# Optimization experiments

Measured on AMD Instinct MI355X. Metric: run time of the kernel, lower is better.

Reference implementation:

```python
import jax, jax.numpy as jnp
import numpy as np

# Module config (matches init_kwargs)
N_HEADS = 16
HEAD = 64
SEQ = 4096          # single prefill sequence (cu_seqlens_k = [0, SEQ])
BS = 64             # block_size (both q and k blocks)
LOCAL = 8           # local_blocks
VERT = 8            # vert_stride
NB = SEQ // BS      # number of blocks along seq
SLIDE = max(1, VERT // N_HEADS)  # get_head_sliding_step(16, 8, homo_head=False) -> 1
SM_SCALE = 1.0 / float(np.sqrt(HEAD))


def _build_layout():
    """Per-head block-sparse layout: causal + (local OR strided-vertical) blocks,
    padded to a fixed max nnz per row (CSR rows -> padded col indices + valid mask)."""
    h = np.arange(N_HEADS)[:, None, None]
    i = np.arange(NB)[None, :, None]
    j = np.arange(NB)[None, None, :]
    mask = (j <= i) & (((i - j) < LOCAL) | (((j + h * SLIDE + 1) % VERT) == 0))
    max_nnz = int(mask.sum(-1).max())
    cols = np.zeros((N_HEADS, NB, max_nnz), np.int32)
    valid = np.zeros((N_HEADS, NB, max_nnz), bool)
    for hh in range(N_HEADS):
        for ii in range(NB):
            c = np.nonzero(mask[hh, ii])[0]
            cols[hh, ii, :len(c)] = c
            valid[hh, ii, :len(c)] = True
    return cols, valid, max_nnz

_COLS_NP, _VALID_NP, MAX_NNZ = _build_layout()
COLS = jnp.asarray(_COLS_NP)    # [H, NB, NNZ] k-block ids (padded with 0)
VALID = jnp.asarray(_VALID_NP)  # [H, NB, NNZ] padding mask


def setup_inputs() -> dict:
    key = jax.random.key(0)
    kq, kk, kv = jax.random.split(key, 3)
    q = jax.random.normal(kq, (SEQ, N_HEADS, HEAD), jnp.float32)
    k = jax.random.normal(kk, (SEQ, N_HEADS, HEAD), jnp.float32)
    v = jax.random.normal(kv, (SEQ, N_HEADS, HEAD), jnp.float32)
    cu_seqlens_k = jnp.array([0, SEQ], jnp.int32)
    return {"q": q, "k": k, "v": v, "cu_seqlens_k": cu_seqlens_k}


def _attn(q, k, v):
    # [T, H, D] -> [H, NB, BS, D]
    qb = q.transpose(1, 0, 2).reshape(N_HEADS, NB, BS, HEAD)
    kb = k.transpose(1, 0, 2).reshape(N_HEADS, NB, BS, HEAD)
    vb = v.transpose(1, 0, 2).reshape(N_HEADS, NB, BS, HEAD)
    gather = jax.vmap(lambda x, c: x[c])  # per-head block gather
    kg = gather(kb, COLS)  # [H, NB, NNZ, BS, D]
    vg = gather(vb, COLS)  # [H, NB, NNZ, BS, D]
    # block-sparse scores: [H, NB(q blk), BS(m), NNZ(n), BS(j)]
    scores = jnp.einsum('himd,hinjd->himnj', qb, kg) * SM_SCALE
    qpos = jnp.arange(NB)[:, None] * BS + jnp.arange(BS)[None, :]   # [NB, BS]
    kpos = COLS[..., None] * BS + jnp.arange(BS)                    # [H, NB, NNZ, BS]
    allow = VALID[:, :, None, :, None] & (
        qpos[None, :, :, None, None] >= kpos[:, :, None, :, :])
    scores = jnp.where(allow, scores, -jnp.inf)
    p = jax.nn.softmax(scores.reshape(N_HEADS, NB, BS, MAX_NNZ * BS), axis=-1)
    p = p.reshape(N_HEADS, NB, BS, MAX_NNZ, BS)
    out = jnp.einsum('himnj,hinjd->himd', p, vg)
    return out.reshape(N_HEADS, SEQ, HEAD).transpose(1, 0, 2)  # [T, H, D]


def reference(q, k, v, cu_seqlens_k):
    # single-sequence prefill: past_len = 0, q_len == k_len == SEQ
    return _attn(q, k, v)
```

## Files before the change

### kernel.cpp

```cpp
#include <hip/hip_runtime.h>
#include <hip/hip_bf16.h>
#include <math.h>


#define NHEADS 16
#define HDIM   64
#define NBLK   64
#define SEQLEN 4096
#define KP     72
#define NEGBIG (-1.0e30f)

typedef __attribute__((ext_vector_type(8))) short bf16x8;
typedef __attribute__((ext_vector_type(4))) float f32x4;

__device__ __forceinline__ short f2bf(float x) {
    union { float f; unsigned u; } c; c.f = x;
    unsigned u = c.u;
    return (short)((u + 0x7FFFu + ((u >> 16) & 1u)) >> 16);
}
__device__ __forceinline__ short f2bf_trunc(float x) {
    union { float f; unsigned u; } c; c.f = x;
    return (short)(c.u >> 16);
}

__device__ __forceinline__ void load_lds16(const short* g, const short* l) {
    __builtin_amdgcn_global_load_lds(
        (const __attribute__((address_space(1))) void*)g,
        (__attribute__((address_space(3))) void*)l, 16, 0, 0);
}

__device__ __forceinline__ void drain_then_sync() {
    asm volatile("s_waitcnt vmcnt(0)" ::: "memory");
    __syncthreads();
}

__global__ __launch_bounds__(256)
void prep_kernel(const float* __restrict__ k, const float* __restrict__ v,
                 short* __restrict__ kt, short* __restrict__ vt) {
    __shared__ short tile[64 * KP];
    const int b = blockIdx.x;
    const int h = b >> 6, jb = b & 63;
    const int tid = threadIdx.x;

    #pragma unroll
    for (int it = 0; it < 4; ++it) {
        int e = it * 1024 + tid * 4;
        int key = e >> 6, d0 = e & 63;
        float4 f = *(const float4*)(v + ((size_t)(jb * 64 + key) * NHEADS + h) * HDIM + d0);
        tile[(d0 + 0) * KP + key] = f2bf(f.x);
        tile[(d0 + 1) * KP + key] = f2bf(f.y);
        tile[(d0 + 2) * KP + key] = f2bf(f.z);
        tile[(d0 + 3) * KP + key] = f2bf(f.w);
    }
    __syncthreads();
    short* vtile = vt + (size_t)b * 4096;
    #pragma unroll
    for (int ii = 0; ii < 2; ++ii) {
        int idx = ii * 256 + tid;
        int d = idx >> 3, gsw = idx & 7;
        int g = gsw ^ (d & 7);
        bf16x8 val;
        #pragma unroll
        for (int j = 0; j < 8; ++j) {
            int s   = g * 8 + j;
            int key = (s & 32) | (((s >> 2) & 1) << 4) | (((s >> 3) & 3) << 2) | (s & 3);
            val[j]  = tile[d * KP + key];
        }
        *(bf16x8*)(vtile + (size_t)idx * 8) = val;
    }
    short* ktile = kt + (size_t)b * 4096;
    #pragma unroll
    for (int ii = 0; ii < 2; ++ii) {
        int idx = ii * 256 + tid;
        int r = idx >> 3, g = idx & 7;
        const float* src = k + ((size_t)(jb * 64 + r) * NHEADS + h) * HDIM + g * 8;
        float4 f0 = *(const float4*)src;
        float4 f1 = *(const float4*)(src + 4);
        bf16x8 a;
        a[0]=f2bf(f0.x); a[1]=f2bf(f0.y); a[2]=f2bf(f0.z); a[3]=f2bf(f0.w);
        a[4]=f2bf(f1.x); a[5]=f2bf(f1.y); a[6]=f2bf(f1.z); a[7]=f2bf(f1.w);
        int G = r * 8 + (g ^ (r & 7));
        *(bf16x8*)(ktile + (size_t)G * 8) = a;
    }
}

__global__ __launch_bounds__(256, 4)
void attn_kernel(const short* __restrict__ kt, const short* __restrict__ vt,
                 const float* __restrict__ q, float* __restrict__ out) {
    __shared__ short kv[2 * 8192];

    const int b    = blockIdx.x;
    const int h    = ((b & 7) << 1) | ((b >> 3) & 1);
    const int idx  = b >> 4;
    const int qi   = (idx & 1) ? (63 - (idx >> 1)) : (idx >> 1);
    const int tid  = threadIdx.x;
    const int stripe = tid >> 6;
    const int lane = tid & 63;
    const int l16  = lane & 15;
    const int quad = lane >> 4;

    const int row0 = qi * 64 + stripe * 16;

    const float SC = 0.125f * 1.4426950408889634f;
    const float* qrow = q + ((size_t)(row0 + l16) * NHEADS + h) * HDIM;
    bf16x8 a_q[2];
    #pragma unroll
    for (int kk = 0; kk < 2; ++kk) {
        const float* src = qrow + kk * 32 + quad * 8;
        float4 f0 = *(const float4*)(src);
        float4 f1 = *(const float4*)(src + 4);
        bf16x8 a;
        a[0]=f2bf(f0.x*SC); a[1]=f2bf(f0.y*SC); a[2]=f2bf(f0.z*SC); a[3]=f2bf(f0.w*SC);
        a[4]=f2bf(f1.x*SC); a[5]=f2bf(f1.y*SC); a[6]=f2bf(f1.z*SC); a[7]=f2bf(f1.w*SC);
        a_q[kk] = a;
    }

    bf16x8 ones;
    #pragma unroll
    for (int j = 0; j < 8; ++j) ones[j] = (short)0x3F80;

    f32x4 o[4];
    #pragma unroll
    for (int nt = 0; nt < 4; ++nt) o[nt] = (f32x4){0.f,0.f,0.f,0.f};
    f32x4 lacc = (f32x4){0.f,0.f,0.f,0.f};

    const short* kth = kt + (size_t)(h * 64) * 4096;
    const short* vth = vt + (size_t)(h * 64) * 4096;

    const int j0  = (7 - h) & 7;
    const int l0  = (qi > 7) ? (qi - 7) : 0;
    const int nv  = (j0 < l0) ? ((l0 - j0 + 7) >> 3) : 0;
    const int T   = nv + (qi - l0 + 1);

    const int r7   = l16 & 7;
    const int gk0  = (quad ^ r7) * 8;
    const int gk1  = gk0 ^ 32;
    const int rowb = l16 * 64;
    const int qrl  = stripe * 16 + l16;

    {
        const int jb0 = (0 < nv) ? j0 : l0;
        const short* ktb = kth + (size_t)jb0 * 4096;
        const short* vtb = vth + (size_t)jb0 * 4096;
        load_lds16(ktb + (size_t)tid * 8,         &kv[stripe * 512]);
        load_lds16(ktb + (size_t)(tid + 256) * 8, &kv[2048 + stripe * 512]);
        load_lds16(vtb + (size_t)tid * 8,         &kv[4096 + stripe * 512]);
        load_lds16(vtb + (size_t)(tid + 256) * 8, &kv[6144 + stripe * 512]);
    }

    for (int t = 0; t < T; ++t) {
        drain_then_sync();

        if (t + 1 < T) {
            const int jn = (t + 1 < nv) ? (j0 + 8 * (t + 1)) : (l0 + (t + 1 - nv));
            const int bo = ((t + 1) & 1) * 8192;
            const short* ktb = kth + (size_t)jn * 4096;
            const short* vtb = vth + (size_t)jn * 4096;
            load_lds16(ktb + (size_t)tid * 8,         &kv[bo + stripe * 512]);
            load_lds16(ktb + (size_t)(tid + 256) * 8, &kv[bo + 2048 + stripe * 512]);
            load_lds16(vtb + (size_t)tid * 8,         &kv[bo + 4096 + stripe * 512]);
            load_lds16(vtb + (size_t)(tid + 256) * 8, &kv[bo + 6144 + stripe * 512]);
        }

        const short* kb = &kv[(t & 1) * 8192];
        const short* vb = kb + 4096;
        const bool diag = (t == T - 1);

        __builtin_amdgcn_s_setprio(1);

        f32x4 s[4];
        #pragma unroll
        for (int nt = 0; nt < 4; ++nt) {
            bf16x8 k0 = *(const bf16x8*)&kb[nt * 1024 + rowb + gk0];
            bf16x8 k1 = *(const bf16x8*)&kb[nt * 1024 + rowb + gk1];
            f32x4 acc = (f32x4){0.f, 0.f, 0.f, 0.f};
            acc = __builtin_amdgcn_mfma_f32_16x16x32_bf16(k0, a_q[0], acc, 0, 0, 0);
            acc = __builtin_amdgcn_mfma_f32_16x16x32_bf16(k1, a_q[1], acc, 0, 0, 0);
            s[nt] = acc;
        }

        short pb[4][4];
        #pragma unroll
        for (int nt = 0; nt < 4; ++nt) {
            #pragma unroll
            for (int r = 0; r < 4; ++r) {
                const int keyl = nt * 16 + quad * 4 + r;
                float raw = s[nt][r];
                raw = (diag && (keyl > qrl)) ? NEGBIG : raw;
                float pv = __builtin_amdgcn_exp2f(raw);
                pb[nt][r] = f2bf_trunc(pv);
            }
        }

        bf16x8 a_p0, a_p1;
        a_p0[0]=pb[0][0]; a_p0[1]=pb[0][1]; a_p0[2]=pb[0][2]; a_p0[3]=pb[0][3];
        a_p0[4]=pb[1][0]; a_p0[5]=pb[1][1]; a_p0[6]=pb[1][2]; a_p0[7]=pb[1][3];
        a_p1[0]=pb[2][0]; a_p1[1]=pb[2][1]; a_p1[2]=pb[2][2]; a_p1[3]=pb[2][3];
        a_p1[4]=pb[3][0]; a_p1[5]=pb[3][1]; a_p1[6]=pb[3][2]; a_p1[7]=pb[3][3];

        #pragma unroll
        for (int nt = 0; nt < 4; ++nt) {
            bf16x8 v0 = *(const bf16x8*)&vb[nt * 1024 + rowb + gk0];
            bf16x8 v1 = *(const bf16x8*)&vb[nt * 1024 + rowb + gk1];
            o[nt] = __builtin_amdgcn_mfma_f32_16x16x32_bf16(a_p0, v0, o[nt], 0, 0, 0);
            o[nt] = __builtin_amdgcn_mfma_f32_16x16x32_bf16(a_p1, v1, o[nt], 0, 0, 0);
        }
        lacc = __builtin_amdgcn_mfma_f32_16x16x32_bf16(a_p0, ones, lacc, 0, 0, 0);
        lacc = __builtin_amdgcn_mfma_f32_16x16x32_bf16(a_p1, ones, lacc, 0, 0, 0);

        __builtin_amdgcn_s_setprio(0);
    }

    #pragma unroll
    for (int r = 0; r < 4; ++r) {
        const float invr = 1.0f / lacc[r];
        int trow = row0 + quad * 4 + r;
        float* orow = out + ((size_t)trow * NHEADS + h) * HDIM;
        #pragma unroll
        for (int nt = 0; nt < 4; ++nt)
            orow[nt * 16 + l16] = o[nt][r] * invr;
    }
}

extern "C" void kernel_launch(void* const* d_in, const int* in_sizes, int n_in,
                              void* d_out, int out_size, void* d_ws, size_t ws_size,
                              hipStream_t stream) {
    const float* q = (const float*)d_in[0];
    const float* k = (const float*)d_in[1];
    const float* v = (const float*)d_in[2];
    float* out = (float*)d_out;

    const size_t tileBytes = (size_t)NHEADS * NBLK * 4096 * sizeof(short);
    short* kt = (short*)d_ws;
    short* vt = (short*)((char*)d_ws + tileBytes);
    prep_kernel<<<dim3(NHEADS * NBLK), dim3(256), 0, stream>>>(k, v, kt, vt);
    attn_kernel<<<dim3(1024), dim3(256), 0, stream>>>(kt, vt, q, out);
}
```

Measured before the change: 110.8 us.

## Split attention tile 2x2 across waves with LDS reduction of partial outputs

Each of the four waves now handles 32 query rows and half of the 64 keys of every block, instead of 16 query rows and all keys. Each wave loads half as many K and V fragments from LDS per block and reuses each one across two query row groups. Partial outputs and row sums from the two key halves are added through LDS in an epilogue. The price is more accumulator registers per wave, extra barriers, and a final reduction in which only half the waves write the output.

```diff
diff --git a/kernel.cpp b/kernel.cpp
--- a/kernel.cpp
+++ b/kernel.cpp
@@ -87,42 +87,51 @@
 __global__ __launch_bounds__(256, 4)
 void attn_kernel(const short* __restrict__ kt, const short* __restrict__ vt,
                  const float* __restrict__ q, float* __restrict__ out) {
-    __shared__ short kv[2 * 8192];
+    __shared__ __align__(16) short kv[2 * 8192];
 
     const int b    = blockIdx.x;
     const int h    = ((b & 7) << 1) | ((b >> 3) & 1);
     const int idx  = b >> 4;
     const int qi   = (idx & 1) ? (63 - (idx >> 1)) : (idx >> 1);
     const int tid  = threadIdx.x;
-    const int stripe = tid >> 6;
+    const int wave = tid >> 6;
+    const int ih   = wave >> 1;
+    const int jh   = wave & 1;
     const int lane = tid & 63;
     const int l16  = lane & 15;
     const int quad = lane >> 4;
 
-    const int row0 = qi * 64 + stripe * 16;
+    const int rowbase = qi * 64 + ih * 32;
 
     const float SC = 0.125f * 1.4426950408889634f;
-    const float* qrow = q + ((size_t)(row0 + l16) * NHEADS + h) * HDIM;
-    bf16x8 a_q[2];
-    #pragma unroll
-    for (int kk = 0; kk < 2; ++kk) {
-        const float* src = qrow + kk * 32 + quad * 8;
-        float4 f0 = *(const float4*)(src);
-        float4 f1 = *(const float4*)(src + 4);
-        bf16x8 a;
-        a[0]=f2bf(f0.x*SC); a[1]=f2bf(f0.y*SC); a[2]=f2bf(f0.z*SC); a[3]=f2bf(f0.w*SC);
-        a[4]=f2bf(f1.x*SC); a[5]=f2bf(f1.y*SC); a[6]=f2bf(f1.z*SC); a[7]=f2bf(f1.w*SC);
-        a_q[kk] = a;
+    bf16x8 a_q[2][2];
+    #pragma unroll
+    for (int rg = 0; rg < 2; ++rg) {
+        const float* qrow = q + ((size_t)(rowbase + rg * 16 + l16) * NHEADS + h) * HDIM;
+        #pragma unroll
+        for (int kk = 0; kk < 2; ++kk) {
+            const float* src = qrow + kk * 32 + quad * 8;
+            float4 f0 = *(const float4*)(src);
+            float4 f1 = *(const float4*)(src + 4);
+            bf16x8 a;
+            a[0]=f2bf(f0.x*SC); a[1]=f2bf(f0.y*SC); a[2]=f2bf(f0.z*SC); a[3]=f2bf(f0.w*SC);
+            a[4]=f2bf(f1.x*SC); a[5]=f2bf(f1.y*SC); a[6]=f2bf(f1.z*SC); a[7]=f2bf(f1.w*SC);
+            a_q[rg][kk] = a;
+        }
     }
 
     bf16x8 ones;
     #pragma unroll
     for (int j = 0; j < 8; ++j) ones[j] = (short)0x3F80;
 
-    f32x4 o[4];
-    #pragma unroll
-    for (int nt = 0; nt < 4; ++nt) o[nt] = (f32x4){0.f,0.f,0.f,0.f};
-    f32x4 lacc = (f32x4){0.f,0.f,0.f,0.f};
+    f32x4 o[2][4];
+    f32x4 lacc[2];
+    #pragma unroll
+    for (int rg = 0; rg < 2; ++rg) {
+        lacc[rg] = (f32x4){0.f,0.f,0.f,0.f};
+        #pragma unroll
+        for (int ntd = 0; ntd < 4; ++ntd) o[rg][ntd] = (f32x4){0.f,0.f,0.f,0.f};
+    }
 
     const short* kth = kt + (size_t)(h * 64) * 4096;
     const short* vth = vt + (size_t)(h * 64) * 4096;
@@ -135,17 +144,18 @@
     const int r7   = l16 & 7;
     const int gk0  = (quad ^ r7) * 8;
     const int gk1  = gk0 ^ 32;
+    const int gv   = (((jh << 2) | quad) ^ r7) * 8;
     const int rowb = l16 * 64;
-    const int qrl  = stripe * 16 + l16;
+    const int krow0 = (jh * 32) * 64;
 
     {
         const int jb0 = (0 < nv) ? j0 : l0;
         const short* ktb = kth + (size_t)jb0 * 4096;
         const short* vtb = vth + (size_t)jb0 * 4096;
-        load_lds16(ktb + (size_t)tid * 8,         &kv[stripe * 512]);
-        load_lds16(ktb + (size_t)(tid + 256) * 8, &kv[2048 + stripe * 512]);
-        load_lds16(vtb + (size_t)tid * 8,         &kv[4096 + stripe * 512]);
-        load_lds16(vtb + (size_t)(tid + 256) * 8, &kv[6144 + stripe * 512]);
+        load_lds16(ktb + (size_t)tid * 8,         &kv[wave * 512]);
+        load_lds16(ktb + (size_t)(tid + 256) * 8, &kv[2048 + wave * 512]);
+        load_lds16(vtb + (size_t)tid * 8,         &kv[4096 + wave * 512]);
+        load_lds16(vtb + (size_t)(tid + 256) * 8, &kv[6144 + wave * 512]);
     }
 
     for (int t = 0; t < T; ++t) {
@@ -156,10 +166,10 @@
             const int bo = ((t + 1) & 1) * 8192;
             const short* ktb = kth + (size_t)jn * 4096;
             const short* vtb = vth + (size_t)jn * 4096;
-            load_lds16(ktb + (size_t)tid * 8,         &kv[bo + stripe * 512]);
-            load_lds16(ktb + (size_t)(tid + 256) * 8, &kv[bo + 2048 + stripe * 512]);
-            load_lds16(vtb + (size_t)tid * 8,         &kv[bo + 4096 + stripe * 512]);
-            load_lds16(vtb + (size_t)(tid + 256) * 8, &kv[bo + 6144 + stripe * 512]);
+            load_lds16(ktb + (size_t)tid * 8,         &kv[bo + wave * 512]);
+            load_lds16(ktb + (size_t)(tid + 256) * 8, &kv[bo + 2048 + wave * 512]);
+            load_lds16(vtb + (size_t)tid * 8,         &kv[bo + 4096 + wave * 512]);
+            load_lds16(vtb + (size_t)(tid + 256) * 8, &kv[bo + 6144 + wave * 512]);
         }
 
         const short* kb = &kv[(t & 1) * 8192];
@@ -168,57 +178,98 @@
 
         __builtin_amdgcn_s_setprio(1);
 
-        f32x4 s[4];
-        #pragma unroll
-        for (int nt = 0; nt < 4; ++nt) {
-            bf16x8 k0 = *(const bf16x8*)&kb[nt * 1024 + rowb + gk0];
-            bf16x8 k1 = *(const bf16x8*)&kb[nt * 1024 + rowb + gk1];
-            f32x4 acc = (f32x4){0.f, 0.f, 0.f, 0.f};
-            acc = __builtin_amdgcn_mfma_f32_16x16x32_bf16(k0, a_q[0], acc, 0, 0, 0);
-            acc = __builtin_amdgcn_mfma_f32_16x16x32_bf16(k1, a_q[1], acc, 0, 0, 0);
-            s[nt] = acc;
-        }
-
-        short pb[4][4];
-        #pragma unroll
-        for (int nt = 0; nt < 4; ++nt) {
+        bf16x8 kf0[2], kf1[2];
+        #pragma unroll
+        for (int kg = 0; kg < 2; ++kg) {
+            kf0[kg] = *(const bf16x8*)&kb[krow0 + kg * 1024 + rowb + gk0];
+            kf1[kg] = *(const bf16x8*)&kb[krow0 + kg * 1024 + rowb + gk1];
+        }
+        f32x4 s[2][2];
+        #pragma unroll
+        for (int kg = 0; kg < 2; ++kg) {
+            #pragma unroll
+            for (int rg = 0; rg < 2; ++rg) {
+                f32x4 acc = (f32x4){0.f, 0.f, 0.f, 0.f};
+                acc = __builtin_amdgcn_mfma_f32_16x16x32_bf16(kf0[kg], a_q[rg][0], acc, 0, 0, 0);
+                acc = __builtin_amdgcn_mfma_f32_16x16x32_bf16(kf1[kg], a_q[rg][1], acc, 0, 0, 0);
+                s[kg][rg] = acc;
+            }
+        }
+
+        bf16x8 vf[4];
+        #pragma unroll
+        for (int ntd = 0; ntd < 4; ++ntd)
+            vf[ntd] = *(const bf16x8*)&vb[ntd * 1024 + rowb + gv];
+
+        short pb[2][2][4];
+        #pragma unroll
+        for (int kg = 0; kg < 2; ++kg) {
+            #pragma unroll
+            for (int rg = 0; rg < 2; ++rg) {
+                #pragma unroll
+                for (int r = 0; r < 4; ++r) {
+                    const int keyl = jh * 32 + kg * 16 + quad * 4 + r;
+                    const int qrl  = ih * 32 + rg * 16 + l16;
+                    float raw = s[kg][rg][r];
+                    raw = (diag && (keyl > qrl)) ? NEGBIG : raw;
+                    float pv = __builtin_amdgcn_exp2f(raw);
+                    pb[kg][rg][r] = f2bf_trunc(pv);
+                }
+            }
+        }
+
+        bf16x8 a_p[2];
+        #pragma unroll
+        for (int rg = 0; rg < 2; ++rg) {
+            bf16x8 a;
+            a[0]=pb[0][rg][0]; a[1]=pb[0][rg][1]; a[2]=pb[0][rg][2]; a[3]=pb[0][rg][3];
+            a[4]=pb[1][rg][0]; a[5]=pb[1][rg][1]; a[6]=pb[1][rg][2]; a[7]=pb[1][rg][3];
+            a_p[rg] = a;
+        }
+
+        #pragma unroll
+        for (int rg = 0; rg < 2; ++rg) {
+            #pragma unroll
+            for (int ntd = 0; ntd < 4; ++ntd)
+                o[rg][ntd] = __builtin_amdgcn_mfma_f32_16x16x32_bf16(a_p[rg], vf[ntd], o[rg][ntd], 0, 0, 0);
+            lacc[rg] = __builtin_amdgcn_mfma_f32_16x16x32_bf16(a_p[rg], ones, lacc[rg], 0, 0, 0);
+        }
+
+        __builtin_amdgcn_s_setprio(0);
+    }
+
+    __syncthreads();
+    f32x4* kvF = (f32x4*)kv;
+    if (jh == 1) {
+        #pragma unroll
+        for (int rg = 0; rg < 2; ++rg) {
+            #pragma unroll
+            for (int ntd = 0; ntd < 4; ++ntd)
+                kvF[(ih * 10 + rg * 4 + ntd) * 64 + lane] = o[rg][ntd];
+            kvF[(ih * 10 + 8 + rg) * 64 + lane] = lacc[rg];
+        }
+    }
+    __syncthreads();
+    if (jh == 0) {
+        #pragma unroll
+        for (int rg = 0; rg < 2; ++rg) {
+            #pragma unroll
+            for (int ntd = 0; ntd < 4; ++ntd)
+                o[rg][ntd] += kvF[(ih * 10 + rg * 4 + ntd) * 64 + lane];
+            lacc[rg] += kvF[(ih * 10 + 8 + rg) * 64 + lane];
+        }
+        #pragma unroll
+        for (int rg = 0; rg < 2; ++rg) {
             #pragma unroll
             for (int r = 0; r < 4; ++r) {
-                const int keyl = nt * 16 + quad * 4 + r;
-                float raw = s[nt][r];
-                raw = (diag && (keyl > qrl)) ? NEGBIG : raw;
-                float pv = __builtin_amdgcn_exp2f(raw);
-                pb[nt][r] = f2bf_trunc(pv);
+                const float invr = 1.0f / lacc[rg][r];
+                int trow = rowbase + rg * 16 + quad * 4 + r;
+                float* orow = out + ((size_t)trow * NHEADS + h) * HDIM;
+                #pragma unroll
+                for (int ntd = 0; ntd < 4; ++ntd)
+                    orow[ntd * 16 + l16] = o[rg][ntd][r] * invr;
             }
         }
-
-        bf16x8 a_p0, a_p1;
-        a_p0[0]=pb[0][0]; a_p0[1]=pb[0][1]; a_p0[2]=pb[0][2]; a_p0[3]=pb[0][3];
-        a_p0[4]=pb[1][0]; a_p0[5]=pb[1][1]; a_p0[6]=pb[1][2]; a_p0[7]=pb[1][3];
-        a_p1[0]=pb[2][0]; a_p1[1]=pb[2][1]; a_p1[2]=pb[2][2]; a_p1[3]=pb[2][3];
-        a_p1[4]=pb[3][0]; a_p1[5]=pb[3][1]; a_p1[6]=pb[3][2]; a_p1[7]=pb[3][3];
-
-        #pragma unroll
-        for (int nt = 0; nt < 4; ++nt) {
-            bf16x8 v0 = *(const bf16x8*)&vb[nt * 1024 + rowb + gk0];
-            bf16x8 v1 = *(const bf16x8*)&vb[nt * 1024 + rowb + gk1];
-            o[nt] = __builtin_amdgcn_mfma_f32_16x16x32_bf16(a_p0, v0, o[nt], 0, 0, 0);
-            o[nt] = __builtin_amdgcn_mfma_f32_16x16x32_bf16(a_p1, v1, o[nt], 0, 0, 0);
-        }
-        lacc = __builtin_amdgcn_mfma_f32_16x16x32_bf16(a_p0, ones, lacc, 0, 0, 0);
-        lacc = __builtin_amdgcn_mfma_f32_16x16x32_bf16(a_p1, ones, lacc, 0, 0, 0);
-
-        __builtin_amdgcn_s_setprio(0);
-    }
-
-    #pragma unroll
-    for (int r = 0; r < 4; ++r) {
-        const float invr = 1.0f / lacc[r];
-        int trow = row0 + quad * 4 + r;
-        float* orow = out + ((size_t)trow * NHEADS + h) * HDIM;
-        #pragma unroll
-        for (int nt = 0; nt < 4; ++nt)
-            orow[nt * 16 + l16] = o[nt][r] * invr;
     }
 }
 
```

After: 111.7 us. No clear change (+0.9%).
